# Kernel optimization log

Measured on AMD Instinct MI355X. Metric: run time of the kernel, lower is better.

The kernel has to match this reference:

```python
import jax, jax.numpy as jnp
import numpy as np

N = 100_000   # nodes
E = 3_200_000 # edges (avg degree 32)
IN = 256      # input feature dim


def setup_inputs() -> dict:
    key = jax.random.key(0)
    ks = jax.random.split(key, 10)
    w = lambda k, s: (jax.random.normal(k, s, jnp.float32) * 0.02)
    return {
        "x": jax.random.normal(ks[0], (N, IN), jnp.float32),
        "edge_index": jax.random.randint(ks[1], (2, E), 0, N, dtype=jnp.int32),
        "edge_attr": jax.random.normal(ks[2], (E, 1), jnp.float32),
        # conv1: ExpGraphConv(IN, 64, 128)
        "W1a": w(ks[3], (IN, 64)), "b1a": jnp.zeros((64,), jnp.float32),
        "W1b": w(ks[4], (IN + 64, 128)), "b1b": jnp.zeros((128,), jnp.float32),
        # conv2: ExpGraphConv(128, 32->hidden 64? per ctor (128, 32, 64)): msg hidden 32... kept as repo: hidden=32? Using (128,64) msg, (192,64) out per faithful cat structure
        "W2a": w(ks[5], (128, 64)), "b2a": jnp.zeros((64,), jnp.float32),
        "W2b": w(ks[6], (128 + 64, 64)), "b2b": jnp.zeros((64,), jnp.float32),
        # head
        "Wl1": w(ks[7], (64, 32)), "bl1": jnp.zeros((32,), jnp.float32),
        "Wl2": w(ks[8], (32, 1)), "bl2": jnp.zeros((1,), jnp.float32),
    }


def _mean_aggr(h, src, dst, n):
    # gather messages from source nodes, scatter-mean into destination nodes
    s = jax.ops.segment_sum(h[src], dst, num_segments=n)          # [N, d]
    cnt = jax.ops.segment_sum(jnp.ones((src.shape[0],), h.dtype), dst, num_segments=n)
    return s / jnp.maximum(cnt, 1.0)[:, None]


def _exp_graph_conv(x, src, dst, Wa, ba, Wb, bb):
    # message MLP on source features, mean aggregation, then linear on [x || aggr]
    h = x @ Wa + ba                                               # [N, hidden]
    m = _mean_aggr(h, src, dst, x.shape[0])                       # [N, hidden]
    return jnp.concatenate([x, m], axis=1) @ Wb + bb              # [N, out]


def reference(x, edge_index, edge_attr, W1a, b1a, W1b, b1b, W2a, b2a, W2b, b2b, Wl1, bl1, Wl2, bl2):
    src, dst = edge_index[0], edge_index[1]
    x = jax.nn.relu(_exp_graph_conv(x, src, dst, W1a, b1a, W1b, b1b))
    x = jax.nn.relu(_exp_graph_conv(x, src, dst, W2a, b2a, W2b, b2b))
    x = jax.nn.relu(x @ Wl1 + bl1)
    return x @ Wl2 + bl2
```

## Files before the change

### kernel.cpp

```cpp
#include <hip/hip_runtime.h>

#define IN_DIM 256
#define CAP 10240
#define EPB 4096

typedef _Float16 f16;
typedef _Float16 f16x8 __attribute__((ext_vector_type(8)));
typedef float f32x4 __attribute__((ext_vector_type(4)));
typedef unsigned u32x4 __attribute__((ext_vector_type(4)));
typedef unsigned u32x2 __attribute__((ext_vector_type(2)));


__global__ __launch_bounds__(256) void bucket_scatter_k(const int* __restrict__ srcp,
                                                        const int* __restrict__ dstp,
                                                        int* __restrict__ bcur,
                                                        unsigned* __restrict__ bedge, int E) {
    __shared__ int cnt[512], lstart[512], delta[512], fill[512];
    __shared__ int pfx[256];
    __shared__ unsigned spay[EPB];
    __shared__ unsigned char sbk[EPB];
    int tid = threadIdx.x;
    cnt[tid] = 0; cnt[tid + 256] = 0;
    fill[tid] = 0; fill[tid + 256] = 0;
    __syncthreads();
    size_t base = (size_t)blockIdx.x * EPB;
    int nloc = E - (int)base; if (nloc > EPB) nloc = EPB;
    int dreg[EPB / 256], sreg[EPB / 256];
#pragma unroll
    for (int j = 0; j < EPB / 256; j++) {
        int e = j * 256 + tid;
        if (e < nloc) {
            dreg[j] = dstp[base + e];
            sreg[j] = srcp[base + e];
            atomicAdd(&cnt[dreg[j] >> 8], 1);
        }
    }
    __syncthreads();
    int a0 = cnt[2 * tid], a1 = cnt[2 * tid + 1], s = a0 + a1;
    pfx[tid] = s;
    __syncthreads();
    for (int off = 1; off < 256; off <<= 1) {
        int t2 = (tid >= off) ? pfx[tid - off] : 0;
        __syncthreads();
        pfx[tid] += t2;
        __syncthreads();
    }
    int excl = pfx[tid] - s;
    lstart[2 * tid] = excl;
    lstart[2 * tid + 1] = excl + a0;
    int g0 = 0, g1 = 0;
    if (a0) g0 = atomicAdd(&bcur[2 * tid], a0);
    if (a1) g1 = atomicAdd(&bcur[2 * tid + 1], a1);
    delta[2 * tid]     = (2 * tid) * CAP + g0 - excl;
    delta[2 * tid + 1] = (2 * tid + 1) * CAP + g1 - (excl + a0);
    __syncthreads();
#pragma unroll
    for (int j = 0; j < EPB / 256; j++) {
        int e = j * 256 + tid;
        if (e < nloc) {
            int d = dreg[j], bk = d >> 8;
            int slot = lstart[bk] + atomicAdd(&fill[bk], 1);
            spay[slot] = (unsigned)sreg[j] | ((unsigned)(d & 255) << 17);
            sbk[slot] = (unsigned char)bk;
        }
    }
    __syncthreads();
    int mid = lstart[256];
#pragma unroll
    for (int j = 0; j < EPB / 256; j++) {
        int i = j * 256 + tid;
        if (i < nloc) {
            int bk = (int)sbk[i] | ((i >= mid) ? 256 : 0);
            int gp = i + delta[bk];
            if (gp < (bk + 1) * CAP)
                bedge[gp] = spay[i];
        }
    }
}

__global__ __launch_bounds__(256) void fine_sort_k(unsigned* __restrict__ bedge,
                                                   const int* __restrict__ bcur,
                                                   int2* __restrict__ ose, int Nn) {
    __shared__ int cnt[256], cur[256], pfx[256];
    __shared__ int sorted[CAP];
    int b = blockIdx.x, tid = threadIdx.x;
    int lo = b * CAP;
    int sz = bcur[b];
    if (sz > CAP) sz = CAP;
    cnt[tid] = 0;
    __syncthreads();
    for (int i = tid; i < sz; i += 256) atomicAdd(&cnt[bedge[lo + i] >> 17], 1);
    __syncthreads();
    int c = cnt[tid];
    pfx[tid] = c;
    __syncthreads();
    for (int off = 1; off < 256; off <<= 1) {
        int t2 = (tid >= off) ? pfx[tid - off] : 0;
        __syncthreads();
        pfx[tid] += t2;
        __syncthreads();
    }
    int excl = pfx[tid] - c;
    cur[tid] = excl;
    int node = b * 256 + tid;
    if (node < Nn) ose[node] = make_int2(lo + excl, lo + excl + c);
    __syncthreads();
    for (int i = tid; i < sz; i += 256) {
        unsigned v = bedge[lo + i];
        int slot = atomicAdd(&cur[v >> 17], 1);
        sorted[slot] = (int)(v & 0x1FFFFu);
    }
    __syncthreads();
    for (int i = tid; i < sz; i += 256) bedge[lo + i] = (unsigned)sorted[i];
}


__global__ __launch_bounds__(256) void wcast_all_k(
    const float* __restrict__ W1a, const float* __restrict__ W1b,
    const float* __restrict__ W2a, const float* __restrict__ W2b,
    const float* __restrict__ b1a, const float* __restrict__ b1b,
    const float* __restrict__ b2a, const float* __restrict__ b2b,
    f16* __restrict__ Wt1, f16* __restrict__ Wm1,
    f16* __restrict__ Wt2, f16* __restrict__ Wm2,
    float* __restrict__ bc1, float* __restrict__ bc2) {
    int i = blockIdx.x * 256 + threadIdx.x;
    if (i < 49152) {
        int n = i >> 8, k = i & 255;
        Wt1[i] = (f16)(n < 64 ? W1a[k * 64 + n] : W1b[k * 128 + (n - 64)]);
    } else if (i < 57344) {
        int l = i - 49152; int n = l >> 6, k = l & 63;
        Wm1[l] = (f16)W1b[(256 + k) * 128 + n];
    } else if (i < 73728) {
        int l = i - 57344; int n = l >> 7, k = l & 127;
        Wt2[l] = (f16)(n < 64 ? W2a[k * 64 + n] : W2b[k * 64 + (n - 64)]);
    } else if (i < 77824) {
        int l = i - 73728; int n = l >> 6, k = l & 63;
        Wm2[l] = (f16)W2b[(128 + k) * 64 + n];
    } else if (i < 78016) {
        int l = i - 77824; bc1[l] = l < 64 ? b1a[l] : b1b[l - 64];
    } else if (i < 78144) {
        int l = i - 78016; bc2[l] = l < 64 ? b2a[l] : b2b[l - 64];
    }
}


template <int BN, bool A1F32>
__global__ __launch_bounds__(256) void gemm_fused(const void* __restrict__ A1v, int K1,
                                                  const f16* __restrict__ Wt,
                                                  const float* __restrict__ bc,
                                                  f16* __restrict__ Y1,
                                                  f16* __restrict__ Y2, int M) {
    constexpr int BM = 64, BK = 32, ASTR = BK + 8;
    constexpr int WN = BN / 2, NB = WN / 16, SEGB = BN / 64;
    constexpr int EPS = BN + 8, TPR = BN / 8, N2 = BN - 64;
    constexpr size_t SM_AB = (size_t)BM * ASTR * 2 + (size_t)BN * ASTR * 2;
    constexpr size_t SM_EP = (size_t)BM * EPS * 2;
    constexpr size_t SM = SM_AB > SM_EP ? SM_AB : SM_EP;
    __shared__ __align__(16) char smem[SM];
    f16* As = reinterpret_cast<f16*>(smem);
    f16* Bs = reinterpret_cast<f16*>(smem + (size_t)BM * ASTR * 2);
    const int tid  = threadIdx.x;
    const int wave = tid >> 6, lane = tid & 63;
    const int wr = wave >> 1, wc = wave & 1;
    const int quad = lane >> 4, l16 = lane & 15;
    const int row0 = blockIdx.x * BM;

    f32x4 acc[2][NB];
#pragma unroll
    for (int i = 0; i < 2; i++)
#pragma unroll
        for (int j = 0; j < NB; j++) acc[i][j] = (f32x4)(0.f);

    const int ra = tid >> 2, sa = tid & 3;
    int rowA = row0 + ra;  if (rowA >= M) rowA = M - 1;

    u32x4 aReg, bReg[SEGB];
    auto loadA = [&](int kk) {
        if constexpr (A1F32) {
            const float* bp = reinterpret_cast<const float*>(A1v) +
                              (size_t)rowA * K1 + kk + sa * 8;
            f32x4 v0 = __builtin_nontemporal_load(reinterpret_cast<const f32x4*>(bp));
            f32x4 v1 = __builtin_nontemporal_load(reinterpret_cast<const f32x4*>(bp) + 1);
            union { f16 h[8]; u32x4 u; } p;
            p.h[0] = (f16)v0.x; p.h[1] = (f16)v0.y; p.h[2] = (f16)v0.z; p.h[3] = (f16)v0.w;
            p.h[4] = (f16)v1.x; p.h[5] = (f16)v1.y; p.h[6] = (f16)v1.z; p.h[7] = (f16)v1.w;
            aReg = p.u;
        } else {
            aReg = __builtin_nontemporal_load(reinterpret_cast<const u32x4*>(
                reinterpret_cast<const f16*>(A1v) + (size_t)rowA * K1 + kk + sa * 8));
        }
    };
    auto loadB = [&](int kk) {
#pragma unroll
        for (int i = 0; i < SEGB; i++) {
            int fid = tid + i * 256;
            int n = fid >> 2, s = fid & 3;
            bReg[i] = *reinterpret_cast<const u32x4*>(Wt + (size_t)n * K1 + kk + s * 8);
        }
    };

    loadA(0); loadB(0);
    for (int kk = 0; kk < K1; kk += BK) {
        *reinterpret_cast<u32x4*>(&As[ra * ASTR + sa * 8]) = aReg;
#pragma unroll
        for (int i = 0; i < SEGB; i++) {
            int fid = tid + i * 256;
            int n = fid >> 2, s = fid & 3;
            *reinterpret_cast<u32x4*>(&Bs[n * ASTR + s * 8]) = bReg[i];
        }
        __syncthreads();
        if (kk + BK < K1) { loadA(kk + BK); loadB(kk + BK); }
        f16x8 af[2], bf[NB];
#pragma unroll
        for (int rb = 0; rb < 2; rb++) {
            int row = wr * 32 + rb * 16 + l16;
            af[rb] = *reinterpret_cast<const f16x8*>(&As[row * ASTR + quad * 8]);
        }
#pragma unroll
        for (int cb = 0; cb < NB; cb++) {
            int n = wc * WN + cb * 16 + l16;
            bf[cb] = *reinterpret_cast<const f16x8*>(&Bs[n * ASTR + quad * 8]);
        }
#pragma unroll
        for (int rb = 0; rb < 2; rb++)
#pragma unroll
            for (int cb = 0; cb < NB; cb++)
                acc[rb][cb] = __builtin_amdgcn_mfma_f32_16x16x32_f16(af[rb], bf[cb], acc[rb][cb], 0, 0, 0);
        __syncthreads();
    }

    f16* ep = reinterpret_cast<f16*>(smem);
#pragma unroll
    for (int rb = 0; rb < 2; rb++) {
#pragma unroll
        for (int cb = 0; cb < NB; cb++) {
            int col = wc * WN + cb * 16 + l16;
            float bv = bc[col];
#pragma unroll
            for (int r = 0; r < 4; r++) {
                int lrow = wr * 32 + rb * 16 + quad * 4 + r;
                ep[(size_t)lrow * EPS + col] = (f16)(acc[rb][cb][r] + bv);
            }
        }
    }
    __syncthreads();
#pragma unroll
    for (int p = 0; p < BM * TPR / 256; p++) {
        int fid = p * 256 + tid;
        int row = fid / TPR, c = fid % TPR, col0 = c * 8;
        int grow = row0 + row;
        if (grow < M) {
            u32x4 val = *reinterpret_cast<const u32x4*>(&ep[(size_t)row * EPS + col0]);
            if (col0 < 64)
                *reinterpret_cast<u32x4*>(Y1 + (size_t)grow * 64 + col0) = val;
            else
                __builtin_nontemporal_store(val,
                    reinterpret_cast<u32x4*>(Y2 + (size_t)grow * N2 + (col0 - 64)));
        }
    }
}


template <int BN, bool FUSE_HEAD>
__global__ __launch_bounds__(256) void agemm(const int2* __restrict__ ose,
                                             const int* __restrict__ ssrc,
                                             const f16* __restrict__ h,
                                             const f16* __restrict__ Wm,
                                             const f16* __restrict__ P,
                                             f16* __restrict__ Y,
                                             const float* __restrict__ Wl1,
                                             const float* __restrict__ bl1,
                                             const float* __restrict__ Wl2,
                                             const float* __restrict__ bl2,
                                             float* __restrict__ out, int M) {
    constexpr int BM = 64, ASTR = 72;
    constexpr int WN = BN / 2, NB = WN / 16;
    constexpr int EPS = BN + 8, TPR = BN / 8;
    constexpr size_t SZ_A = (size_t)BM * ASTR * 2;
    constexpr size_t SM_AB = SZ_A + (size_t)BN * ASTR * 2;
    constexpr size_t SM_EP = (size_t)BM * EPS * 2;
    constexpr size_t SM_CORE = SM_AB > SM_EP ? SM_AB : SM_EP;
    constexpr size_t SM_HEAD = FUSE_HEAD ? (2048 + 64) * 4 : 0;
    __shared__ __align__(16) char smem[SM_CORE + SM_HEAD];
    f16* Am = reinterpret_cast<f16*>(smem);
    f16* Bs = reinterpret_cast<f16*>(smem + SZ_A);
    const int tid  = threadIdx.x;
    const int wave = tid >> 6, lane = tid & 63;
    const int wr = wave >> 1, wc = wave & 1;
    const int quad = lane >> 4, l16 = lane & 15;
    const int row0 = blockIdx.x * BM;

    for (int fid = tid; fid < BN * 8; fid += 256) {
        int n = fid >> 3, s = fid & 7;
        *reinterpret_cast<u32x4*>(&Bs[n * ASTR + s * 8]) =
            *reinterpret_cast<const u32x4*>(Wm + (size_t)n * 64 + s * 8);
    }
    if constexpr (FUSE_HEAD) {
        float* w1s = reinterpret_cast<float*>(smem + SM_CORE);
        for (int t2 = tid; t2 < 2048; t2 += 256) w1s[t2] = Wl1[t2];
        if (tid < 32) { w1s[2048 + tid] = bl1[tid]; w1s[2048 + 32 + tid] = Wl2[tid]; }
    }

    const u32x2* hp = reinterpret_cast<const u32x2*>(h);
    for (int i = 0; i < 16; i++) {
        int node = wave * 16 + i, gnode = row0 + node;
        int s0 = 0, s1 = 0;
        if (gnode < M) { int2 se = ose[gnode]; s0 = se.x; s1 = se.y; }
        float a0 = 0.f, a1 = 0.f, a2 = 0.f, a3 = 0.f;
        auto accum = [&](u32x2 u) {
            union { u32x2 u; f16 hh[4]; } p; p.u = u;
            a0 += (float)p.hh[0]; a1 += (float)p.hh[1];
            a2 += (float)p.hh[2]; a3 += (float)p.hh[3];
        };
        for (int c = s0; c < s1; c += 64) {
            int cn = min(64, s1 - c);
            int myidx = (lane < cn) ? ssrc[c + lane] : 0;
            int t = 0;
            for (; t + 16 <= cn; t += 16) {
                int ia = __shfl(myidx, t + quad);
                int ib = __shfl(myidx, t + 4 + quad);
                int ic = __shfl(myidx, t + 8 + quad);
                int id = __shfl(myidx, t + 12 + quad);
                u32x2 ua = hp[(size_t)ia * 16 + l16];
                u32x2 ub = hp[(size_t)ib * 16 + l16];
                u32x2 uc = hp[(size_t)ic * 16 + l16];
                u32x2 ud = hp[(size_t)id * 16 + l16];
                accum(ua); accum(ub); accum(uc); accum(ud);
            }
            for (; t < cn; t += 4) {
                int r = t + quad;
                int rr = (r < cn) ? r : (cn - 1);
                int ia = __shfl(myidx, rr);
                if (r < cn) accum(hp[(size_t)ia * 16 + l16]);
            }
        }
        a0 += __shfl_xor(a0, 16); a1 += __shfl_xor(a1, 16);
        a2 += __shfl_xor(a2, 16); a3 += __shfl_xor(a3, 16);
        a0 += __shfl_xor(a0, 32); a1 += __shfl_xor(a1, 32);
        a2 += __shfl_xor(a2, 32); a3 += __shfl_xor(a3, 32);
        if (lane < 16) {
            float inv = 1.0f / fmaxf((float)(s1 - s0), 1.0f);
            union { u32x2 u; f16 hh[4]; } pk;
            pk.hh[0] = (f16)(a0 * inv); pk.hh[1] = (f16)(a1 * inv);
            pk.hh[2] = (f16)(a2 * inv); pk.hh[3] = (f16)(a3 * inv);
            *reinterpret_cast<u32x2*>(&Am[node * ASTR + l16 * 4]) = pk.u;
        }
    }
    __syncthreads();

    f32x4 acc[2][NB];
#pragma unroll
    for (int i = 0; i < 2; i++)
#pragma unroll
        for (int j = 0; j < NB; j++) acc[i][j] = (f32x4)(0.f);
#pragma unroll
    for (int ks = 0; ks < 2; ks++) {
        f16x8 af[2], bf[NB];
#pragma unroll
        for (int rb = 0; rb < 2; rb++) {
            int row = wr * 32 + rb * 16 + l16;
            af[rb] = *reinterpret_cast<const f16x8*>(&Am[row * ASTR + ks * 32 + quad * 8]);
        }
#pragma unroll
        for (int cb = 0; cb < NB; cb++) {
            int n = wc * WN + cb * 16 + l16;
            bf[cb] = *reinterpret_cast<const f16x8*>(&Bs[n * ASTR + ks * 32 + quad * 8]);
        }
#pragma unroll
        for (int rb = 0; rb < 2; rb++)
#pragma unroll
            for (int cb = 0; cb < NB; cb++)
                acc[rb][cb] = __builtin_amdgcn_mfma_f32_16x16x32_f16(af[rb], bf[cb], acc[rb][cb], 0, 0, 0);
    }
    __syncthreads();

    f16* ep = reinterpret_cast<f16*>(smem);
#pragma unroll
    for (int rb = 0; rb < 2; rb++) {
#pragma unroll
        for (int cb = 0; cb < NB; cb++) {
            int col = wc * WN + cb * 16 + l16;
#pragma unroll
            for (int r = 0; r < 4; r++) {
                int lrow = wr * 32 + rb * 16 + quad * 4 + r;
                int grow = row0 + lrow;
                float pv = (grow < M) ? (float)P[(size_t)grow * BN + col] : 0.f;
                float v = fmaxf(acc[rb][cb][r] + pv, 0.f);
                ep[(size_t)lrow * EPS + col] = (f16)v;
            }
        }
    }
    __syncthreads();

    if constexpr (FUSE_HEAD) {
        float* w1s = reinterpret_cast<float*>(smem + SM_CORE);
        float* b1s = w1s + 2048;
        float* w2s = b1s + 32;
        int row = tid >> 2, part = tid & 3;
        const f16* eprow = ep + (size_t)row * EPS;
        float hj[8];
#pragma unroll
        for (int j = 0; j < 8; j++) hj[j] = b1s[part * 8 + j];
        for (int k = 0; k < 64; k++) {
            float v = (float)eprow[k];
            const float* wrow = &w1s[k * 32 + part * 8];
#pragma unroll
            for (int j = 0; j < 8; j++) hj[j] += v * wrow[j];
        }
        float o = 0.f;
#pragma unroll
        for (int j = 0; j < 8; j++) o += fmaxf(hj[j], 0.f) * w2s[part * 8 + j];
        o += __shfl_xor(o, 1);
        o += __shfl_xor(o, 2);
        int grow = row0 + row;
        if (part == 0 && grow < M) out[grow] = o + bl2[0];
    } else {
#pragma unroll
        for (int p = 0; p < BM * TPR / 256; p++) {
            int fid = p * 256 + tid;
            int row = fid / TPR, c = fid % TPR;
            int grow = row0 + row;
            if (grow < M) {
                u32x4 val = *reinterpret_cast<const u32x4*>(&ep[(size_t)row * EPS + c * 8]);
                *reinterpret_cast<u32x4*>(Y + (size_t)grow * BN + c * 8) = val;
            }
        }
    }
}


extern "C" void kernel_launch(void* const* d_in, const int* in_sizes, int n_in,
                              void* d_out, int out_size, void* d_ws, size_t ws_size,
                              hipStream_t stream) {
    const float* x   = (const float*)d_in[0];
    const int*   ei  = (const int*)d_in[1];
    const float* W1a = (const float*)d_in[3];
    const float* b1a = (const float*)d_in[4];
    const float* W1b = (const float*)d_in[5];
    const float* b1b = (const float*)d_in[6];
    const float* W2a = (const float*)d_in[7];
    const float* b2a = (const float*)d_in[8];
    const float* W2b = (const float*)d_in[9];
    const float* b2b = (const float*)d_in[10];
    const float* Wl1 = (const float*)d_in[11];
    const float* bl1 = (const float*)d_in[12];
    const float* Wl2 = (const float*)d_in[13];
    const float* bl2 = (const float*)d_in[14];

    const int N = in_sizes[0] / IN_DIM;
    const int E = in_sizes[1] / 2;
    const int* srcp = ei;
    const int* dstp = ei + E;

    char* ws = (char*)d_ws;
    size_t off = 0;
    auto alloc = [&](size_t bytes) -> char* {
        char* p = ws + off;
        off = (off + bytes + 255) & ~(size_t)255;
        return p;
    };
    int NB2 = (N + 255) / 256;
    int*      bcur  = (int*)alloc(512 * 4);
    unsigned* bedge = (unsigned*)alloc((size_t)NB2 * CAP * 4);
    int2*     ose   = (int2*)alloc((size_t)N * 8);
    f16*      hbuf  = (f16*)alloc((size_t)N * 64 * 2);
    f16*      pbuf  = (f16*)alloc((size_t)N * 128 * 2);
    f16*      x1    = (f16*)alloc((size_t)N * 128 * 2);
    f16*      h2    = (f16*)alloc((size_t)N * 64 * 2);
    f16*      p2    = (f16*)alloc((size_t)N * 64 * 2);
    f16*      Wt1   = (f16*)alloc(192 * 256 * 2);
    f16*      Wm1   = (f16*)alloc(128 * 64 * 2);
    f16*      Wt2   = (f16*)alloc(128 * 128 * 2);
    f16*      Wm2   = (f16*)alloc(64 * 64 * 2);
    float*    bc1   = (float*)alloc(192 * 4);
    float*    bc2   = (float*)alloc(128 * 4);
    (void)ws_size;

    hipMemsetAsync(bcur, 0, 512 * 4, stream);
    int ebk = (E + EPB - 1) / EPB;
    bucket_scatter_k<<<ebk, 256, 0, stream>>>(srcp, dstp, bcur, bedge, E);
    fine_sort_k<<<NB2, 256, 0, stream>>>(bedge, bcur, ose, N);

    wcast_all_k<<<306, 256, 0, stream>>>(W1a, W1b, W2a, W2b, b1a, b1b, b2a, b2b,
                                         Wt1, Wm1, Wt2, Wm2, bc1, bc2);

    int mb = (N + 63) / 64;
    const int* ssrc = (const int*)bedge;

    gemm_fused<192, true><<<mb, 256, 0, stream>>>(x, 256, Wt1, bc1, hbuf, pbuf, N);
    agemm<128, false><<<mb, 256, 0, stream>>>(ose, ssrc, hbuf, Wm1, pbuf, x1,
                                              nullptr, nullptr, nullptr, nullptr,
                                              nullptr, N);

    gemm_fused<128, false><<<mb, 256, 0, stream>>>(x1, 128, Wt2, bc2, h2, p2, N);
    agemm<64, true><<<mb, 256, 0, stream>>>(ose, ssrc, h2, Wm2, p2, nullptr,
                                            Wl1, bl1, Wl2, bl2, (float*)d_out, N);
}
```

Measured before the change: 514.0 us.

## Replace MFMA aggregate-GEMM with one-node-per-wave aggregation and scalar matvec

The fused aggregation+GEMM kernel, which used 64-node blocks, a serial per-wave loop over 16 nodes and an MFMA epilogue, is replaced by a kernel that gives each wave a single node. That wave gathers and averages the neighbour features, then computes the 64xNOUT matvec with scalar FMAs against weights cast into shared memory, and applies the optional head. This raises block count and per-wave parallelism for the latency-bound gather, and removes the separate Wm weight-cast work. In exchange, every 4-node block reloads and casts the full Wm (and the head weights) into LDS, and tensor-core use for that product is dropped.

Measured after the change: 526.1 us. 2.4% more time.

```diff
diff --git a/kernel.cpp b/kernel.cpp
--- a/kernel.cpp
+++ b/kernel.cpp
@@ -120,26 +120,19 @@
     const float* __restrict__ W2a, const float* __restrict__ W2b,
     const float* __restrict__ b1a, const float* __restrict__ b1b,
     const float* __restrict__ b2a, const float* __restrict__ b2b,
-    f16* __restrict__ Wt1, f16* __restrict__ Wm1,
-    f16* __restrict__ Wt2, f16* __restrict__ Wm2,
+    f16* __restrict__ Wt1, f16* __restrict__ Wt2,
     float* __restrict__ bc1, float* __restrict__ bc2) {
     int i = blockIdx.x * 256 + threadIdx.x;
     if (i < 49152) {
         int n = i >> 8, k = i & 255;
         Wt1[i] = (f16)(n < 64 ? W1a[k * 64 + n] : W1b[k * 128 + (n - 64)]);
-    } else if (i < 57344) {
-        int l = i - 49152; int n = l >> 6, k = l & 63;
-        Wm1[l] = (f16)W1b[(256 + k) * 128 + n];
-    } else if (i < 73728) {
-        int l = i - 57344; int n = l >> 7, k = l & 127;
+    } else if (i < 65536) {
+        int l = i - 49152; int n = l >> 7, k = l & 127;
         Wt2[l] = (f16)(n < 64 ? W2a[k * 64 + n] : W2b[k * 64 + (n - 64)]);
-    } else if (i < 77824) {
-        int l = i - 73728; int n = l >> 6, k = l & 63;
-        Wm2[l] = (f16)W2b[(128 + k) * 64 + n];
-    } else if (i < 78016) {
-        int l = i - 77824; bc1[l] = l < 64 ? b1a[l] : b1b[l - 64];
-    } else if (i < 78144) {
-        int l = i - 78016; bc2[l] = l < 64 ? b2a[l] : b2b[l - 64];
+    } else if (i < 65728) {
+        int l = i - 65536; bc1[l] = l < 64 ? b1a[l] : b1b[l - 64];
+    } else if (i < 65856) {
+        int l = i - 65728; bc2[l] = l < 64 ? b2a[l] : b2b[l - 64];
     }
 }
 
@@ -261,169 +254,118 @@
 }
 
 
-template <int BN, bool FUSE_HEAD>
-__global__ __launch_bounds__(256) void agemm(const int2* __restrict__ ose,
-                                             const int* __restrict__ ssrc,
-                                             const f16* __restrict__ h,
-                                             const f16* __restrict__ Wm,
-                                             const f16* __restrict__ P,
-                                             f16* __restrict__ Y,
-                                             const float* __restrict__ Wl1,
-                                             const float* __restrict__ bl1,
-                                             const float* __restrict__ Wl2,
-                                             const float* __restrict__ bl2,
-                                             float* __restrict__ out, int M) {
-    constexpr int BM = 64, ASTR = 72;
-    constexpr int WN = BN / 2, NB = WN / 16;
-    constexpr int EPS = BN + 8, TPR = BN / 8;
-    constexpr size_t SZ_A = (size_t)BM * ASTR * 2;
-    constexpr size_t SM_AB = SZ_A + (size_t)BN * ASTR * 2;
-    constexpr size_t SM_EP = (size_t)BM * EPS * 2;
-    constexpr size_t SM_CORE = SM_AB > SM_EP ? SM_AB : SM_EP;
-    constexpr size_t SM_HEAD = FUSE_HEAD ? (2048 + 64) * 4 : 0;
-    __shared__ __align__(16) char smem[SM_CORE + SM_HEAD];
-    f16* Am = reinterpret_cast<f16*>(smem);
-    f16* Bs = reinterpret_cast<f16*>(smem + SZ_A);
-    const int tid  = threadIdx.x;
-    const int wave = tid >> 6, lane = tid & 63;
-    const int wr = wave >> 1, wc = wave & 1;
-    const int quad = lane >> 4, l16 = lane & 15;
-    const int row0 = blockIdx.x * BM;
-
-    for (int fid = tid; fid < BN * 8; fid += 256) {
-        int n = fid >> 3, s = fid & 7;
-        *reinterpret_cast<u32x4*>(&Bs[n * ASTR + s * 8]) =
-            *reinterpret_cast<const u32x4*>(Wm + (size_t)n * 64 + s * 8);
-    }
-    if constexpr (FUSE_HEAD) {
-        float* w1s = reinterpret_cast<float*>(smem + SM_CORE);
-        for (int t2 = tid; t2 < 2048; t2 += 256) w1s[t2] = Wl1[t2];
-        if (tid < 32) { w1s[2048 + tid] = bl1[tid]; w1s[2048 + 32 + tid] = Wl2[tid]; }
-    }
-
+template <int NOUT, bool HEAD>
+__global__ __launch_bounds__(256) void aggrc_k(const int2* __restrict__ ose,
+                                               const int* __restrict__ ssrc,
+                                               const f16* __restrict__ h,
+                                               const float* __restrict__ Wm,
+                                               const f16* __restrict__ P,
+                                               f16* __restrict__ Y,
+                                               const float* __restrict__ Wl1,
+                                               const float* __restrict__ bl1,
+                                               const float* __restrict__ Wl2,
+                                               const float* __restrict__ bl2,
+                                               float* __restrict__ out, int n) {
+    __shared__ f16 wms[64 * NOUT];
+    __shared__ __align__(16) float mrow[4][72];
+    __shared__ float w1s[HEAD ? 2048 : 1];
+    __shared__ float b1s[HEAD ? 32 : 1];
+    __shared__ float w2s[HEAD ? 32 : 1];
+    __shared__ f16 yrow[HEAD ? 4 : 1][72];
+    const int tid = threadIdx.x;
+    for (int i = tid; i < 64 * NOUT; i += 256) wms[i] = (f16)Wm[i];
+    if constexpr (HEAD) {
+        for (int i = tid; i < 2048; i += 256) w1s[i] = Wl1[i];
+        if (tid < 32) { b1s[tid] = bl1[tid]; w2s[tid] = Wl2[tid]; }
+    }
+    __syncthreads();
+
+    const int wv = tid >> 6, lane = tid & 63;
+    const int node = blockIdx.x * 4 + wv;
+    if (node >= n) return;
+    int2 se = ose[node];
+    int s0 = se.x, s1 = se.y;
+    const int q = lane >> 4, l16 = lane & 15;
     const u32x2* hp = reinterpret_cast<const u32x2*>(h);
-    for (int i = 0; i < 16; i++) {
-        int node = wave * 16 + i, gnode = row0 + node;
-        int s0 = 0, s1 = 0;
-        if (gnode < M) { int2 se = ose[gnode]; s0 = se.x; s1 = se.y; }
-        float a0 = 0.f, a1 = 0.f, a2 = 0.f, a3 = 0.f;
-        auto accum = [&](u32x2 u) {
-            union { u32x2 u; f16 hh[4]; } p; p.u = u;
-            a0 += (float)p.hh[0]; a1 += (float)p.hh[1];
-            a2 += (float)p.hh[2]; a3 += (float)p.hh[3];
-        };
-        for (int c = s0; c < s1; c += 64) {
-            int cn = min(64, s1 - c);
-            int myidx = (lane < cn) ? ssrc[c + lane] : 0;
-            int t = 0;
-            for (; t + 16 <= cn; t += 16) {
-                int ia = __shfl(myidx, t + quad);
-                int ib = __shfl(myidx, t + 4 + quad);
-                int ic = __shfl(myidx, t + 8 + quad);
-                int id = __shfl(myidx, t + 12 + quad);
-                u32x2 ua = hp[(size_t)ia * 16 + l16];
-                u32x2 ub = hp[(size_t)ib * 16 + l16];
-                u32x2 uc = hp[(size_t)ic * 16 + l16];
-                u32x2 ud = hp[(size_t)id * 16 + l16];
-                accum(ua); accum(ub); accum(uc); accum(ud);
+    float a0 = 0.f, a1 = 0.f, a2 = 0.f, a3 = 0.f;
+    auto accum = [&](u32x2 u) {
+        union { u32x2 u; f16 hh[4]; } p; p.u = u;
+        a0 += (float)p.hh[0]; a1 += (float)p.hh[1];
+        a2 += (float)p.hh[2]; a3 += (float)p.hh[3];
+    };
+    for (int c = s0; c < s1; c += 64) {
+        int cn = min(64, s1 - c);
+        int myidx = (lane < cn) ? ssrc[c + lane] : 0;
+        int t = 0;
+        for (; t + 16 <= cn; t += 16) {
+            int ia = __shfl(myidx, t + q);
+            int ib = __shfl(myidx, t + 4 + q);
+            int ic = __shfl(myidx, t + 8 + q);
+            int id = __shfl(myidx, t + 12 + q);
+            u32x2 ua = hp[(size_t)ia * 16 + l16];
+            u32x2 ub = hp[(size_t)ib * 16 + l16];
+            u32x2 uc = hp[(size_t)ic * 16 + l16];
+            u32x2 ud = hp[(size_t)id * 16 + l16];
+            accum(ua); accum(ub); accum(uc); accum(ud);
+        }
+        for (; t < cn; t += 4) {
+            int r = t + q;
+            int rr = (r < cn) ? r : (cn - 1);
+            int ia = __shfl(myidx, rr);
+            if (r < cn) accum(hp[(size_t)ia * 16 + l16]);
+        }
+    }
+    a0 += __shfl_xor(a0, 16); a1 += __shfl_xor(a1, 16);
+    a2 += __shfl_xor(a2, 16); a3 += __shfl_xor(a3, 16);
+    a0 += __shfl_xor(a0, 32); a1 += __shfl_xor(a1, 32);
+    a2 += __shfl_xor(a2, 32); a3 += __shfl_xor(a3, 32);
+    float inv = 1.0f / fmaxf((float)(s1 - s0), 1.0f);
+    if (lane < 16) {
+        f32x4 mv; mv.x = a0 * inv; mv.y = a1 * inv; mv.z = a2 * inv; mv.w = a3 * inv;
+        *reinterpret_cast<f32x4*>(&mrow[wv][l16 * 4]) = mv;
+    }
+
+    if constexpr (NOUT == 128) {
+        float acc0 = 0.f, acc1 = 0.f;
+        const unsigned* wmu = reinterpret_cast<const unsigned*>(wms);
+#pragma unroll 8
+        for (int k = 0; k < 64; k++) {
+            float mk = mrow[wv][k];
+            union { unsigned u; f16 hh[2]; } w; w.u = wmu[k * 64 + lane];
+            acc0 += mk * (float)w.hh[0];
+            acc1 += mk * (float)w.hh[1];
+        }
+        union { unsigned u; f16 hh[2]; } pv;
+        pv.u = *reinterpret_cast<const unsigned*>(P + (size_t)node * 128 + 2 * lane);
+        union { unsigned u; f16 hh[2]; } yv;
+        yv.hh[0] = (f16)fmaxf(acc0 + (float)pv.hh[0], 0.f);
+        yv.hh[1] = (f16)fmaxf(acc1 + (float)pv.hh[1], 0.f);
+        *reinterpret_cast<unsigned*>(Y + (size_t)node * 128 + 2 * lane) = yv.u;
+    } else {
+        float acc0 = 0.f;
+#pragma unroll 8
+        for (int k = 0; k < 64; k++) {
+            float mk = mrow[wv][k];
+            acc0 += mk * (float)wms[k * 64 + lane];
+        }
+        float yval = fmaxf(acc0 + (float)P[(size_t)node * 64 + lane], 0.f);
+        if constexpr (HEAD) {
+            yrow[wv][lane] = (f16)yval;
+            if (lane < 32) {
+                float hj = b1s[lane];
+#pragma unroll 8
+                for (int k = 0; k < 64; k++)
+                    hj += (float)yrow[wv][k] * w1s[k * 32 + lane];
+                float o = fmaxf(hj, 0.f) * w2s[lane];
+                o += __shfl_xor(o, 1);
+                o += __shfl_xor(o, 2);
+                o += __shfl_xor(o, 4);
+                o += __shfl_xor(o, 8);
+                o += __shfl_xor(o, 16);
+                if (lane == 0) out[node] = o + bl2[0];
             }
-            for (; t < cn; t += 4) {
-                int r = t + quad;
-                int rr = (r < cn) ? r : (cn - 1);
-                int ia = __shfl(myidx, rr);
-                if (r < cn) accum(hp[(size_t)ia * 16 + l16]);
-            }
-        }
-        a0 += __shfl_xor(a0, 16); a1 += __shfl_xor(a1, 16);
-        a2 += __shfl_xor(a2, 16); a3 += __shfl_xor(a3, 16);
-        a0 += __shfl_xor(a0, 32); a1 += __shfl_xor(a1, 32);
-        a2 += __shfl_xor(a2, 32); a3 += __shfl_xor(a3, 32);
-        if (lane < 16) {
-            float inv = 1.0f / fmaxf((float)(s1 - s0), 1.0f);
-            union { u32x2 u; f16 hh[4]; } pk;
-            pk.hh[0] = (f16)(a0 * inv); pk.hh[1] = (f16)(a1 * inv);
-            pk.hh[2] = (f16)(a2 * inv); pk.hh[3] = (f16)(a3 * inv);
-            *reinterpret_cast<u32x2*>(&Am[node * ASTR + l16 * 4]) = pk.u;
-        }
-    }
-    __syncthreads();
-
-    f32x4 acc[2][NB];
-#pragma unroll
-    for (int i = 0; i < 2; i++)
-#pragma unroll
-        for (int j = 0; j < NB; j++) acc[i][j] = (f32x4)(0.f);
-#pragma unroll
-    for (int ks = 0; ks < 2; ks++) {
-        f16x8 af[2], bf[NB];
-#pragma unroll
-        for (int rb = 0; rb < 2; rb++) {
-            int row = wr * 32 + rb * 16 + l16;
-            af[rb] = *reinterpret_cast<const f16x8*>(&Am[row * ASTR + ks * 32 + quad * 8]);
-        }
-#pragma unroll
-        for (int cb = 0; cb < NB; cb++) {
-            int n = wc * WN + cb * 16 + l16;
-            bf[cb] = *reinterpret_cast<const f16x8*>(&Bs[n * ASTR + ks * 32 + quad * 8]);
-        }
-#pragma unroll
-        for (int rb = 0; rb < 2; rb++)
-#pragma unroll
-            for (int cb = 0; cb < NB; cb++)
-                acc[rb][cb] = __builtin_amdgcn_mfma_f32_16x16x32_f16(af[rb], bf[cb], acc[rb][cb], 0, 0, 0);
-    }
-    __syncthreads();
-
-    f16* ep = reinterpret_cast<f16*>(smem);
-#pragma unroll
-    for (int rb = 0; rb < 2; rb++) {
-#pragma unroll
-        for (int cb = 0; cb < NB; cb++) {
-            int col = wc * WN + cb * 16 + l16;
-#pragma unroll
-            for (int r = 0; r < 4; r++) {
-                int lrow = wr * 32 + rb * 16 + quad * 4 + r;
-                int grow = row0 + lrow;
-                float pv = (grow < M) ? (float)P[(size_t)grow * BN + col] : 0.f;
-                float v = fmaxf(acc[rb][cb][r] + pv, 0.f);
-                ep[(size_t)lrow * EPS + col] = (f16)v;
-            }
-        }
-    }
-    __syncthreads();
-
-    if constexpr (FUSE_HEAD) {
-        float* w1s = reinterpret_cast<float*>(smem + SM_CORE);
-        float* b1s = w1s + 2048;
-        float* w2s = b1s + 32;
-        int row = tid >> 2, part = tid & 3;
-        const f16* eprow = ep + (size_t)row * EPS;
-        float hj[8];
-#pragma unroll
-        for (int j = 0; j < 8; j++) hj[j] = b1s[part * 8 + j];
-        for (int k = 0; k < 64; k++) {
-            float v = (float)eprow[k];
-            const float* wrow = &w1s[k * 32 + part * 8];
-#pragma unroll
-            for (int j = 0; j < 8; j++) hj[j] += v * wrow[j];
-        }
-        float o = 0.f;
-#pragma unroll
-        for (int j = 0; j < 8; j++) o += fmaxf(hj[j], 0.f) * w2s[part * 8 + j];
-        o += __shfl_xor(o, 1);
-        o += __shfl_xor(o, 2);
-        int grow = row0 + row;
-        if (part == 0 && grow < M) out[grow] = o + bl2[0];
-    } else {
-#pragma unroll
-        for (int p = 0; p < BM * TPR / 256; p++) {
-            int fid = p * 256 + tid;
-            int row = fid / TPR, c = fid % TPR;
-            int grow = row0 + row;
-            if (grow < M) {
-                u32x4 val = *reinterpret_cast<const u32x4*>(&ep[(size_t)row * EPS + c * 8]);
-                *reinterpret_cast<u32x4*>(Y + (size_t)grow * BN + c * 8) = val;
-            }
+        } else {
+            Y[(size_t)node * 64 + lane] = (f16)yval;
         }
     }
 }
@@ -469,9 +411,7 @@
     f16*      h2    = (f16*)alloc((size_t)N * 64 * 2);
     f16*      p2    = (f16*)alloc((size_t)N * 64 * 2);
     f16*      Wt1   = (f16*)alloc(192 * 256 * 2);
-    f16*      Wm1   = (f16*)alloc(128 * 64 * 2);
     f16*      Wt2   = (f16*)alloc(128 * 128 * 2);
-    f16*      Wm2   = (f16*)alloc(64 * 64 * 2);
     float*    bc1   = (float*)alloc(192 * 4);
     float*    bc2   = (float*)alloc(128 * 4);
     (void)ws_size;
@@ -481,18 +421,20 @@
     bucket_scatter_k<<<ebk, 256, 0, stream>>>(srcp, dstp, bcur, bedge, E);
     fine_sort_k<<<NB2, 256, 0, stream>>>(bedge, bcur, ose, N);
 
-    wcast_all_k<<<306, 256, 0, stream>>>(W1a, W1b, W2a, W2b, b1a, b1b, b2a, b2b,
-                                         Wt1, Wm1, Wt2, Wm2, bc1, bc2);
+    wcast_all_k<<<258, 256, 0, stream>>>(W1a, W1b, W2a, W2b, b1a, b1b, b2a, b2b,
+                                         Wt1, Wt2, bc1, bc2);
 
     int mb = (N + 63) / 64;
+    int ab = (N + 3) / 4;
     const int* ssrc = (const int*)bedge;
 
     gemm_fused<192, true><<<mb, 256, 0, stream>>>(x, 256, Wt1, bc1, hbuf, pbuf, N);
-    agemm<128, false><<<mb, 256, 0, stream>>>(ose, ssrc, hbuf, Wm1, pbuf, x1,
-                                              nullptr, nullptr, nullptr, nullptr,
-                                              nullptr, N);
+    aggrc_k<128, false><<<ab, 256, 0, stream>>>(ose, ssrc, hbuf, W1b + 256 * 128,
+                                                pbuf, x1, nullptr, nullptr, nullptr,
+                                                nullptr, nullptr, N);
 
     gemm_fused<128, false><<<mb, 256, 0, stream>>>(x1, 128, Wt2, bc2, h2, p2, N);
-    agemm<64, true><<<mb, 256, 0, stream>>>(ose, ssrc, h2, Wm2, p2, nullptr,
-                                            Wl1, bl1, Wl2, bl2, (float*)d_out, N);
-}
+    aggrc_k<64, true><<<ab, 256, 0, stream>>>(ose, ssrc, h2, W2b + 128 * 64,
+                                              p2, nullptr, Wl1, bl1, Wl2, bl2,
+                                              (float*)d_out, N);
+}
```

## Split fused aggregate-GEMM into a per-node aggregation kernel and a combine GEMM

Applied to the files above, without the earlier changes.

The kernel that gathered neighbor features (16 nodes serially per wave) and then ran the MFMA GEMM is split in two. A standalone aggregation kernel now assigns one wave per node and writes the mean to a global buffer, and a combine kernel loads that buffer into shared memory for the GEMM, epilogue and optional head. This exposes far more parallelism and latency hiding for the irregular gather. The cost is an extra launch per layer and a global write and read of an N×64 f16 intermediate.

New measurement: 445.9 us. -13.3%, faster.

```diff
diff --git a/kernel.cpp b/kernel.cpp
--- a/kernel.cpp
+++ b/kernel.cpp
@@ -120,22 +120,22 @@
     const float* __restrict__ W2a, const float* __restrict__ W2b,
     const float* __restrict__ b1a, const float* __restrict__ b1b,
     const float* __restrict__ b2a, const float* __restrict__ b2b,
-    f16* __restrict__ Wt1, f16* __restrict__ Wm1,
-    f16* __restrict__ Wt2, f16* __restrict__ Wm2,
+    f16* __restrict__ Wt1, f16* __restrict__ Wt2,
+    f16* __restrict__ Wmt1, f16* __restrict__ Wmt2,
     float* __restrict__ bc1, float* __restrict__ bc2) {
     int i = blockIdx.x * 256 + threadIdx.x;
     if (i < 49152) {
         int n = i >> 8, k = i & 255;
         Wt1[i] = (f16)(n < 64 ? W1a[k * 64 + n] : W1b[k * 128 + (n - 64)]);
-    } else if (i < 57344) {
-        int l = i - 49152; int n = l >> 6, k = l & 63;
-        Wm1[l] = (f16)W1b[(256 + k) * 128 + n];
+    } else if (i < 65536) {
+        int l = i - 49152; int n = l >> 7, k = l & 127;
+        Wt2[l] = (f16)(n < 64 ? W2a[k * 64 + n] : W2b[k * 64 + (n - 64)]);
     } else if (i < 73728) {
-        int l = i - 57344; int n = l >> 7, k = l & 127;
-        Wt2[l] = (f16)(n < 64 ? W2a[k * 64 + n] : W2b[k * 64 + (n - 64)]);
+        int l = i - 65536; int n = l >> 6, k = l & 63;
+        Wmt1[l] = (f16)W1b[(256 + k) * 128 + n];
     } else if (i < 77824) {
         int l = i - 73728; int n = l >> 6, k = l & 63;
-        Wm2[l] = (f16)W2b[(128 + k) * 64 + n];
+        Wmt2[l] = (f16)W2b[(128 + k) * 64 + n];
     } else if (i < 78016) {
         int l = i - 77824; bc1[l] = l < 64 ? b1a[l] : b1b[l - 64];
     } else if (i < 78144) {
@@ -261,18 +261,69 @@
 }
 
 
-template <int BN, bool FUSE_HEAD>
-__global__ __launch_bounds__(256) void agemm(const int2* __restrict__ ose,
-                                             const int* __restrict__ ssrc,
-                                             const f16* __restrict__ h,
-                                             const f16* __restrict__ Wm,
-                                             const f16* __restrict__ P,
-                                             f16* __restrict__ Y,
-                                             const float* __restrict__ Wl1,
-                                             const float* __restrict__ bl1,
-                                             const float* __restrict__ Wl2,
-                                             const float* __restrict__ bl2,
-                                             float* __restrict__ out, int M) {
+__global__ __launch_bounds__(256) void aggr_k(const int2* __restrict__ ose,
+                                              const int* __restrict__ ssrc,
+                                              const f16* __restrict__ h,
+                                              f16* __restrict__ m, int n) {
+    int wave = (blockIdx.x * 256 + threadIdx.x) >> 6;
+    int lane = threadIdx.x & 63;
+    if (wave >= n) return;
+    int2 se = ose[wave];
+    int s0 = se.x, s1 = se.y;
+    int q = lane >> 4, l16 = lane & 15;
+    const u32x2* hp = reinterpret_cast<const u32x2*>(h);
+    float a0 = 0.f, a1 = 0.f, a2 = 0.f, a3 = 0.f;
+    auto acc = [&](u32x2 u) {
+        union { u32x2 u; f16 hh[4]; } p; p.u = u;
+        a0 += (float)p.hh[0]; a1 += (float)p.hh[1];
+        a2 += (float)p.hh[2]; a3 += (float)p.hh[3];
+    };
+    for (int c = s0; c < s1; c += 64) {
+        int cn = min(64, s1 - c);
+        int myidx = (lane < cn) ? ssrc[c + lane] : 0;
+        int t = 0;
+        for (; t + 16 <= cn; t += 16) {
+            int ia = __shfl(myidx, t + q);
+            int ib = __shfl(myidx, t + 4 + q);
+            int ic = __shfl(myidx, t + 8 + q);
+            int id = __shfl(myidx, t + 12 + q);
+            u32x2 ua = hp[(size_t)ia * 16 + l16];
+            u32x2 ub = hp[(size_t)ib * 16 + l16];
+            u32x2 uc = hp[(size_t)ic * 16 + l16];
+            u32x2 ud = hp[(size_t)id * 16 + l16];
+            acc(ua); acc(ub); acc(uc); acc(ud);
+        }
+        for (; t < cn; t += 4) {
+            int r = t + q;
+            int rr = (r < cn) ? r : (cn - 1);
+            int ia = __shfl(myidx, rr);
+            if (r < cn) acc(hp[(size_t)ia * 16 + l16]);
+        }
+    }
+    a0 += __shfl_xor(a0, 16); a1 += __shfl_xor(a1, 16);
+    a2 += __shfl_xor(a2, 16); a3 += __shfl_xor(a3, 16);
+    a0 += __shfl_xor(a0, 32); a1 += __shfl_xor(a1, 32);
+    a2 += __shfl_xor(a2, 32); a3 += __shfl_xor(a3, 32);
+    if (lane < 16) {
+        float inv = 1.0f / fmaxf((float)(s1 - s0), 1.0f);
+        union { u32x2 u; f16 hh[4]; } p;
+        p.hh[0] = (f16)(a0 * inv); p.hh[1] = (f16)(a1 * inv);
+        p.hh[2] = (f16)(a2 * inv); p.hh[3] = (f16)(a3 * inv);
+        reinterpret_cast<u32x2*>(m + (size_t)wave * 64)[l16] = p.u;
+    }
+}
+
+
+template <int BN, bool HEAD>
+__global__ __launch_bounds__(256) void combine_k(const f16* __restrict__ Mb,
+                                                 const f16* __restrict__ Wmt,
+                                                 const f16* __restrict__ P,
+                                                 f16* __restrict__ Y,
+                                                 const float* __restrict__ Wl1,
+                                                 const float* __restrict__ bl1,
+                                                 const float* __restrict__ Wl2,
+                                                 const float* __restrict__ bl2,
+                                                 float* __restrict__ out, int M) {
     constexpr int BM = 64, ASTR = 72;
     constexpr int WN = BN / 2, NB = WN / 16;
     constexpr int EPS = BN + 8, TPR = BN / 8;
@@ -280,9 +331,9 @@
     constexpr size_t SM_AB = SZ_A + (size_t)BN * ASTR * 2;
     constexpr size_t SM_EP = (size_t)BM * EPS * 2;
     constexpr size_t SM_CORE = SM_AB > SM_EP ? SM_AB : SM_EP;
-    constexpr size_t SM_HEAD = FUSE_HEAD ? (2048 + 64) * 4 : 0;
+    constexpr size_t SM_HEAD = HEAD ? (2048 + 64) * 4 : 0;
     __shared__ __align__(16) char smem[SM_CORE + SM_HEAD];
-    f16* Am = reinterpret_cast<f16*>(smem);
+    f16* As = reinterpret_cast<f16*>(smem);
     f16* Bs = reinterpret_cast<f16*>(smem + SZ_A);
     const int tid  = threadIdx.x;
     const int wave = tid >> 6, lane = tid & 63;
@@ -290,62 +341,23 @@
     const int quad = lane >> 4, l16 = lane & 15;
     const int row0 = blockIdx.x * BM;
 
+#pragma unroll
+    for (int fid = tid; fid < 512; fid += 256) {
+        int row = fid >> 3, s = fid & 7;
+        int grow = row0 + row; if (grow >= M) grow = M - 1;
+        *reinterpret_cast<u32x4*>(&As[row * ASTR + s * 8]) =
+            *reinterpret_cast<const u32x4*>(Mb + (size_t)grow * 64 + s * 8);
+    }
     for (int fid = tid; fid < BN * 8; fid += 256) {
         int n = fid >> 3, s = fid & 7;
         *reinterpret_cast<u32x4*>(&Bs[n * ASTR + s * 8]) =
-            *reinterpret_cast<const u32x4*>(Wm + (size_t)n * 64 + s * 8);
-    }
-    if constexpr (FUSE_HEAD) {
+            *reinterpret_cast<const u32x4*>(Wmt + (size_t)n * 64 + s * 8);
+    }
+    if constexpr (HEAD) {
         float* w1s = reinterpret_cast<float*>(smem + SM_CORE);
         for (int t2 = tid; t2 < 2048; t2 += 256) w1s[t2] = Wl1[t2];
         if (tid < 32) { w1s[2048 + tid] = bl1[tid]; w1s[2048 + 32 + tid] = Wl2[tid]; }
     }
-
-    const u32x2* hp = reinterpret_cast<const u32x2*>(h);
-    for (int i = 0; i < 16; i++) {
-        int node = wave * 16 + i, gnode = row0 + node;
-        int s0 = 0, s1 = 0;
-        if (gnode < M) { int2 se = ose[gnode]; s0 = se.x; s1 = se.y; }
-        float a0 = 0.f, a1 = 0.f, a2 = 0.f, a3 = 0.f;
-        auto accum = [&](u32x2 u) {
-            union { u32x2 u; f16 hh[4]; } p; p.u = u;
-            a0 += (float)p.hh[0]; a1 += (float)p.hh[1];
-            a2 += (float)p.hh[2]; a3 += (float)p.hh[3];
-        };
-        for (int c = s0; c < s1; c += 64) {
-            int cn = min(64, s1 - c);
-            int myidx = (lane < cn) ? ssrc[c + lane] : 0;
-            int t = 0;
-            for (; t + 16 <= cn; t += 16) {
-                int ia = __shfl(myidx, t + quad);
-                int ib = __shfl(myidx, t + 4 + quad);
-                int ic = __shfl(myidx, t + 8 + quad);
-                int id = __shfl(myidx, t + 12 + quad);
-                u32x2 ua = hp[(size_t)ia * 16 + l16];
-                u32x2 ub = hp[(size_t)ib * 16 + l16];
-                u32x2 uc = hp[(size_t)ic * 16 + l16];
-                u32x2 ud = hp[(size_t)id * 16 + l16];
-                accum(ua); accum(ub); accum(uc); accum(ud);
-            }
-            for (; t < cn; t += 4) {
-                int r = t + quad;
-                int rr = (r < cn) ? r : (cn - 1);
-                int ia = __shfl(myidx, rr);
-                if (r < cn) accum(hp[(size_t)ia * 16 + l16]);
-            }
-        }
-        a0 += __shfl_xor(a0, 16); a1 += __shfl_xor(a1, 16);
-        a2 += __shfl_xor(a2, 16); a3 += __shfl_xor(a3, 16);
-        a0 += __shfl_xor(a0, 32); a1 += __shfl_xor(a1, 32);
-        a2 += __shfl_xor(a2, 32); a3 += __shfl_xor(a3, 32);
-        if (lane < 16) {
-            float inv = 1.0f / fmaxf((float)(s1 - s0), 1.0f);
-            union { u32x2 u; f16 hh[4]; } pk;
-            pk.hh[0] = (f16)(a0 * inv); pk.hh[1] = (f16)(a1 * inv);
-            pk.hh[2] = (f16)(a2 * inv); pk.hh[3] = (f16)(a3 * inv);
-            *reinterpret_cast<u32x2*>(&Am[node * ASTR + l16 * 4]) = pk.u;
-        }
-    }
     __syncthreads();
 
     f32x4 acc[2][NB];
@@ -359,7 +371,7 @@
 #pragma unroll
         for (int rb = 0; rb < 2; rb++) {
             int row = wr * 32 + rb * 16 + l16;
-            af[rb] = *reinterpret_cast<const f16x8*>(&Am[row * ASTR + ks * 32 + quad * 8]);
+            af[rb] = *reinterpret_cast<const f16x8*>(&As[row * ASTR + ks * 32 + quad * 8]);
         }
 #pragma unroll
         for (int cb = 0; cb < NB; cb++) {
@@ -392,7 +404,7 @@
     }
     __syncthreads();
 
-    if constexpr (FUSE_HEAD) {
+    if constexpr (HEAD) {
         float* w1s = reinterpret_cast<float*>(smem + SM_CORE);
         float* b1s = w1s + 2048;
         float* w2s = b1s + 32;
@@ -464,14 +476,15 @@
     unsigned* bedge = (unsigned*)alloc((size_t)NB2 * CAP * 4);
     int2*     ose   = (int2*)alloc((size_t)N * 8);
     f16*      hbuf  = (f16*)alloc((size_t)N * 64 * 2);
+    f16*      mbuf  = (f16*)alloc((size_t)N * 64 * 2);
     f16*      pbuf  = (f16*)alloc((size_t)N * 128 * 2);
     f16*      x1    = (f16*)alloc((size_t)N * 128 * 2);
     f16*      h2    = (f16*)alloc((size_t)N * 64 * 2);
     f16*      p2    = (f16*)alloc((size_t)N * 64 * 2);
     f16*      Wt1   = (f16*)alloc(192 * 256 * 2);
-    f16*      Wm1   = (f16*)alloc(128 * 64 * 2);
     f16*      Wt2   = (f16*)alloc(128 * 128 * 2);
-    f16*      Wm2   = (f16*)alloc(64 * 64 * 2);
+    f16*      Wmt1  = (f16*)alloc(128 * 64 * 2);
+    f16*      Wmt2  = (f16*)alloc(64 * 64 * 2);
     float*    bc1   = (float*)alloc(192 * 4);
     float*    bc2   = (float*)alloc(128 * 4);
     (void)ws_size;
@@ -482,17 +495,20 @@
     fine_sort_k<<<NB2, 256, 0, stream>>>(bedge, bcur, ose, N);
 
     wcast_all_k<<<306, 256, 0, stream>>>(W1a, W1b, W2a, W2b, b1a, b1b, b2a, b2b,
-                                         Wt1, Wm1, Wt2, Wm2, bc1, bc2);
+                                         Wt1, Wt2, Wmt1, Wmt2, bc1, bc2);
 
     int mb = (N + 63) / 64;
+    int ab = (N * 64 + 255) / 256;
     const int* ssrc = (const int*)bedge;
 
     gemm_fused<192, true><<<mb, 256, 0, stream>>>(x, 256, Wt1, bc1, hbuf, pbuf, N);
-    agemm<128, false><<<mb, 256, 0, stream>>>(ose, ssrc, hbuf, Wm1, pbuf, x1,
-                                              nullptr, nullptr, nullptr, nullptr,
-                                              nullptr, N);
+    aggr_k<<<ab, 256, 0, stream>>>(ose, ssrc, hbuf, mbuf, N);
+    combine_k<128, false><<<mb, 256, 0, stream>>>(mbuf, Wmt1, pbuf, x1,
+                                                  nullptr, nullptr, nullptr, nullptr,
+                                                  nullptr, N);
 
     gemm_fused<128, false><<<mb, 256, 0, stream>>>(x1, 128, Wt2, bc2, h2, p2, N);
-    agemm<64, true><<<mb, 256, 0, stream>>>(ose, ssrc, h2, Wm2, p2, nullptr,
-                                            Wl1, bl1, Wl2, bl2, (float*)d_out, N);
-}
+    aggr_k<<<ab, 256, 0, stream>>>(ose, ssrc, h2, mbuf, N);
+    combine_k<64, true><<<mb, 256, 0, stream>>>(mbuf, Wmt2, p2, nullptr,
+                                                Wl1, bl1, Wl2, bl2, (float*)d_out, N);
+}
```
